# Kernel optimization log

Measured on AMD Instinct MI355X. Metric: run time of the kernel, lower is better.

Reference implementation:

```python
import jax, jax.numpy as jnp
import numpy as np

N_NODES = 200_000
N_EDGES = 6_400_000
N_GRAPHS = 512


def _sage_conv(x, edge_index, Wl, bl, Wr):
    """PyG SAGEConv (mean aggr): lin_l(mean_j x_j) + lin_r(x_i).
    lin_l has bias, lin_r does not. Messages flow src -> dst."""
    src, dst = edge_index[0], edge_index[1]
    n = x.shape[0]
    # gather neighbor features [E, F] and segment-mean into dst nodes
    msg_sum = jax.ops.segment_sum(x[src], dst, num_segments=n)
    deg = jax.ops.segment_sum(jnp.ones((src.shape[0],), x.dtype), dst, num_segments=n)
    mean = msg_sum / jnp.maximum(deg, 1.0)[:, None]  # zero in-degree -> 0
    return mean @ Wl.T + bl + x @ Wr.T


def setup_inputs() -> dict:
    key = jax.random.key(0)
    ks = jax.random.split(key, 9)
    x = jax.random.normal(ks[0], (N_NODES, 1), dtype=jnp.float32)
    edge_index = jax.random.randint(ks[1], (2, N_EDGES), 0, N_NODES, dtype=jnp.int64)
    batch = jnp.sort(jax.random.randint(ks[2], (N_NODES,), 0, N_GRAPHS, dtype=jnp.int64))
    W1l = jax.random.normal(ks[3], (16, 1), dtype=jnp.float32)
    b1 = jax.random.normal(ks[4], (16,), dtype=jnp.float32)
    W1r = jax.random.normal(ks[5], (16, 1), dtype=jnp.float32)
    W2l = jax.random.normal(ks[6], (1, 16), dtype=jnp.float32)
    b2 = jax.random.normal(ks[7], (1,), dtype=jnp.float32)
    W2r = jax.random.normal(ks[8], (1, 16), dtype=jnp.float32)
    return {"x": x, "edge_index": edge_index, "batch": batch, "batch_size": N_GRAPHS,
            "W1l": W1l, "b1": b1, "W1r": W1r, "W2l": W2l, "b2": b2, "W2r": W2r}


def reference(x, edge_index, batch, batch_size, W1l, b1, W1r, W2l, b2, W2r):
    h = _sage_conv(x, edge_index, W1l, b1, W1r)          # [N, 16]
    h = jax.nn.relu(h)
    h = _sage_conv(h, edge_index, W2l, b2, W2r)          # [N, 1]
    # global_add_pool: segment-sum node features by graph id
    out = jax.ops.segment_sum(h, batch, num_segments=batch_size)  # [B, 1]
    return out
```

## Files before the change

### kernel.cpp

```cpp
#include <hip/hip_runtime.h>


#define PP        16
#define BLK       1024
#define SCAP      1024u
#define SMASK     1023u
#define TILE      (BLK * 4)
#define CBIN      16
#define CNT_ONE   (1u << 25)
#define FX_BIAS   131072
#define SCALE     4096.0f
#define INV_SCALE (1.0f / 4096.0f)

__global__ __launch_bounds__(BLK) void partition_kernel(
    const int* __restrict__ ei, unsigned* __restrict__ pairs,
    unsigned* __restrict__ tails, int E, int bins, unsigned Mdiv, int cap) {
    extern __shared__ unsigned buf[];
    __shared__ unsigned cnt[PP], base[PP], fq[PP], gb[PP];
    const int tid = threadIdx.x;
    if (tid < PP) { cnt[tid] = 0; base[tid] = 0; }
    __syncthreads();

    int b0 = blockIdx.x * TILE;
    int e0 = b0 + tid * 4;
    int nv = E - e0; nv = nv < 0 ? 0 : (nv > 4 ? 4 : nv);
    int srcv[4], dstv[4];
    if (nv == 4 && ((E & 3) == 0)) {
        int4 s = *(const int4*)(ei + e0);
        int4 d = *(const int4*)(ei + E + e0);
        srcv[0] = s.x; srcv[1] = s.y; srcv[2] = s.z; srcv[3] = s.w;
        dstv[0] = d.x; dstv[1] = d.y; dstv[2] = d.z; dstv[3] = d.w;
    } else {
        for (int j = 0; j < nv; ++j) { srcv[j] = ei[e0 + j]; dstv[j] = ei[E + e0 + j]; }
    }
    unsigned w[4]; int part[4]; bool pend[4];
    for (int j = 0; j < 4; ++j) {
        pend[j] = (j < nv);
        if (pend[j]) {
            unsigned dst = (unsigned)dstv[j];
            unsigned pt = (unsigned)(((unsigned long long)dst * Mdiv) >> 32);
            int ld = (int)dst - (int)pt * bins;
            while (ld >= bins) { ld -= bins; ++pt; }
            while (ld < 0)     { ld += bins; --pt; }
            part[j] = (int)pt;
            w[j] = ((unsigned)srcv[j] << 14) | (unsigned)ld;
        }
    }
    for (int j = 0; j < 4; ++j) {
        if (pend[j]) {
            unsigned slot = atomicAdd(&cnt[part[j]], 1u);
            if (slot - base[part[j]] < SCAP) {
                buf[part[j] * SCAP + (slot & SMASK)] = w[j]; pend[j] = false;
            } else atomicSub(&cnt[part[j]], 1u);
        }
    }
    int npend = __syncthreads_count((int)(pend[0] | pend[1] | pend[2] | pend[3]));
    while (npend > 0) {
        if (tid < PP) {
            unsigned avail = cnt[tid] - base[tid];
            unsigned f = avail & ~511u;
            fq[tid] = f;
            if (f) gb[tid] = atomicAdd(&tails[tid], f);
        }
        __syncthreads();
        {
            int wv = tid >> 6, lane = tid & 63;
            unsigned f = fq[wv];
            if (f) {
                unsigned g0 = gb[wv], bs = base[wv];
                unsigned mx = (g0 + f <= (unsigned)cap) ? f : ((unsigned)cap > g0 ? (unsigned)cap - g0 : 0u);
                unsigned* dp = pairs + (size_t)wv * cap + g0;
                for (unsigned jj = lane; jj < mx; jj += 64)
                    dp[jj] = buf[wv * SCAP + ((bs + jj) & SMASK)];
            }
        }
        __syncthreads();
        if (tid < PP) base[tid] += fq[tid];
        __syncthreads();
        for (int j = 0; j < 4; ++j) {
            if (pend[j]) {
                unsigned slot = atomicAdd(&cnt[part[j]], 1u);
                if (slot - base[part[j]] < SCAP) {
                    buf[part[j] * SCAP + (slot & SMASK)] = w[j]; pend[j] = false;
                } else atomicSub(&cnt[part[j]], 1u);
            }
        }
        npend = __syncthreads_count((int)(pend[0] | pend[1] | pend[2] | pend[3]));
    }
    if (tid < PP) {
        unsigned avail = cnt[tid] - base[tid];
        fq[tid] = avail;
        if (avail) gb[tid] = atomicAdd(&tails[tid], avail);
    }
    __syncthreads();
    {
        int wv = tid >> 6, lane = tid & 63;
        unsigned f = fq[wv];
        if (f) {
            unsigned g0 = gb[wv], bs = base[wv];
            unsigned mx = (g0 + f <= (unsigned)cap) ? f : ((unsigned)cap > g0 ? (unsigned)cap - g0 : 0u);
            unsigned* dp = pairs + (size_t)wv * cap + g0;
            for (unsigned jj = lane; jj < mx; jj += 64)
                dp[jj] = buf[wv * SCAP + ((bs + jj) & SMASK)];
        }
    }
}

__global__ __launch_bounds__(BLK) void bin1_kernel(
    const unsigned* __restrict__ pairs, const unsigned* __restrict__ tails,
    const float* __restrict__ x, unsigned* __restrict__ slab,
    int N, int bins, int cap) {
    extern __shared__ unsigned sb[];
    int p = blockIdx.x & (PP - 1);
    int c = blockIdx.x / PP;
    int len = (int)tails[p]; if (len > cap) len = cap;
    int st = (int)((long long)len * c / CBIN);
    int en = (int)((long long)len * (c + 1) / CBIN);
    for (int j = threadIdx.x; j < bins; j += BLK) sb[j] = 0;
    __syncthreads();
    const unsigned* bp = pairs + (size_t)p * cap;
    int st4 = (st + 3) & ~3;
    int en4 = en & ~3;
    int preEnd = st4 < en ? st4 : en;
    for (int e = st + (int)threadIdx.x; e < preEnd; e += BLK) {
        unsigned wv = bp[e];
        atomicAdd(&sb[wv & 16383u],
                  CNT_ONE + (unsigned)((int)rintf(x[wv >> 14] * SCALE) + FX_BIAS));
    }
    if (st4 < en4) {
        const uint4* bp4 = (const uint4*)(bp + st4);
        int n4 = (en4 - st4) >> 2;
        for (int e = threadIdx.x; e < n4; e += BLK) {
            uint4 wq = bp4[e];
            atomicAdd(&sb[wq.x & 16383u],
                      CNT_ONE + (unsigned)((int)rintf(x[wq.x >> 14] * SCALE) + FX_BIAS));
            atomicAdd(&sb[wq.y & 16383u],
                      CNT_ONE + (unsigned)((int)rintf(x[wq.y >> 14] * SCALE) + FX_BIAS));
            atomicAdd(&sb[wq.z & 16383u],
                      CNT_ONE + (unsigned)((int)rintf(x[wq.z >> 14] * SCALE) + FX_BIAS));
            atomicAdd(&sb[wq.w & 16383u],
                      CNT_ONE + (unsigned)((int)rintf(x[wq.w >> 14] * SCALE) + FX_BIAS));
        }
    }
    int tailSt = st4 > en4 ? st4 : en4;
    for (int e = tailSt + (int)threadIdx.x; e < en; e += BLK) {
        unsigned wv = bp[e];
        atomicAdd(&sb[wv & 16383u],
                  CNT_ONE + (unsigned)((int)rintf(x[wv >> 14] * SCALE) + FX_BIAS));
    }
    __syncthreads();
    unsigned* dst = slab + (size_t)c * N + (size_t)p * bins;
    int nb = N - p * bins; if (nb > bins) nb = bins;
    for (int j = threadIdx.x; j < nb; j += BLK) dst[j] = sb[j];
}

__global__ __launch_bounds__(BLK) void bin2_kernel(
    const unsigned* __restrict__ pairs, const unsigned* __restrict__ tails,
    const float* __restrict__ pv, int* __restrict__ slab,
    int N, int bins, int cap) {
    extern __shared__ int sbi[];
    int p = blockIdx.x & (PP - 1);
    int c = blockIdx.x / PP;
    int len = (int)tails[p]; if (len > cap) len = cap;
    int st = (int)((long long)len * c / CBIN);
    int en = (int)((long long)len * (c + 1) / CBIN);
    for (int j = threadIdx.x; j < bins; j += BLK) sbi[j] = 0;
    __syncthreads();
    const unsigned* bp = pairs + (size_t)p * cap;
    int st4 = (st + 3) & ~3;
    int en4 = en & ~3;
    int preEnd = st4 < en ? st4 : en;
    for (int e = st + (int)threadIdx.x; e < preEnd; e += BLK) {
        unsigned wv = bp[e];
        atomicAdd(&sbi[wv & 16383u], (int)rintf(pv[wv >> 14] * SCALE));
    }
    if (st4 < en4) {
        const uint4* bp4 = (const uint4*)(bp + st4);
        int n4 = (en4 - st4) >> 2;
        for (int e = threadIdx.x; e < n4; e += BLK) {
            uint4 wq = bp4[e];
            atomicAdd(&sbi[wq.x & 16383u], (int)rintf(pv[wq.x >> 14] * SCALE));
            atomicAdd(&sbi[wq.y & 16383u], (int)rintf(pv[wq.y >> 14] * SCALE));
            atomicAdd(&sbi[wq.z & 16383u], (int)rintf(pv[wq.z >> 14] * SCALE));
            atomicAdd(&sbi[wq.w & 16383u], (int)rintf(pv[wq.w >> 14] * SCALE));
        }
    }
    int tailSt = st4 > en4 ? st4 : en4;
    for (int e = tailSt + (int)threadIdx.x; e < en; e += BLK) {
        unsigned wv = bp[e];
        atomicAdd(&sbi[wv & 16383u], (int)rintf(pv[wv >> 14] * SCALE));
    }
    __syncthreads();
    int* dst = slab + (size_t)c * N + (size_t)p * bins;
    int nb = N - p * bins; if (nb > bins) nb = bins;
    for (int j = threadIdx.x; j < nb; j += BLK) dst[j] = sbi[j];
}

__global__ void node_pass1_kernel(const float* __restrict__ x,
                                  const unsigned* __restrict__ slab,
                                  const float* __restrict__ W1l,
                                  const float* __restrict__ b1,
                                  const float* __restrict__ W1r,
                                  const float* __restrict__ W2l,
                                  const float* __restrict__ W2r,
                                  float* __restrict__ deg_out,
                                  float* __restrict__ pv,
                                  float* __restrict__ qv,
                                  int N) {
    __shared__ float s_w1l[16], s_b1[16], s_w1r[16], s_w2l[16], s_w2r[16];
    if (threadIdx.x < 16) {
        s_w1l[threadIdx.x] = W1l[threadIdx.x];
        s_b1[threadIdx.x]  = b1[threadIdx.x];
        s_w1r[threadIdx.x] = W1r[threadIdx.x];
        s_w2l[threadIdx.x] = W2l[threadIdx.x];
        s_w2r[threadIdx.x] = W2r[threadIdx.x];
    }
    __syncthreads();
    int n = blockIdx.x * blockDim.x + threadIdx.x;
    if (n >= N) return;

    unsigned cnt = 0, fx = 0;
#pragma unroll
    for (int c = 0; c < CBIN; ++c) {
        unsigned w = slab[(size_t)c * N + n];
        cnt += w >> 25;
        fx  += w & (CNT_ONE - 1);
    }
    float dg  = (float)cnt;
    float sum = (float)(int)(fx - cnt * (unsigned)FX_BIAS) * INV_SCALE;
    float m   = sum / fmaxf(dg, 1.0f);

    float xv = x[n];
    float pa = 0.0f, qa = 0.0f;
#pragma unroll
    for (int f = 0; f < 16; ++f) {
        float h = fmaf(m, s_w1l[f], fmaf(xv, s_w1r[f], s_b1[f]));
        h = fmaxf(h, 0.0f);
        pa = fmaf(h, s_w2l[f], pa);
        qa = fmaf(h, s_w2r[f], qa);
    }
    deg_out[n] = dg;
    pv[n] = pa;
    qv[n] = qa;
}

__global__ void node_pass2_kernel(const int* __restrict__ slab2,
                                  const float* __restrict__ deg,
                                  const float* __restrict__ qv,
                                  const float* __restrict__ b2,
                                  const int* __restrict__ batch,
                                  float* __restrict__ out,
                                  int N) {
    int i = blockIdx.x * blockDim.x + threadIdx.x;
    float b2v = b2[0];
    float val = 0.0f;
    int g;
    if (i < N) {
        int sacc = 0;
#pragma unroll
        for (int c = 0; c < CBIN; ++c) sacc += slab2[(size_t)c * N + i];
        float s2 = (float)sacc * INV_SCALE;
        val = s2 / fmaxf(deg[i], 1.0f) + b2v + qv[i];
        g = batch[i];
    } else {
        g = batch[N - 1];
    }
    int g0 = __shfl(g, 0);
    unsigned long long same = __ballot(g == g0);
    if (same == ~0ULL) {
        for (int off = 32; off > 0; off >>= 1) val += __shfl_down(val, off);
        if ((threadIdx.x & 63) == 0) atomicAdd(&out[g0], val);
    } else {
        atomicAdd(&out[g], val);
    }
}

extern "C" void kernel_launch(void* const* d_in, const int* in_sizes, int n_in,
                              void* d_out, int out_size, void* d_ws, size_t ws_size,
                              hipStream_t stream) {
    const float* x     = (const float*)d_in[0];
    const int*   ei    = (const int*)d_in[1];
    const int*   batch = (const int*)d_in[2];
    const float* W1l = (const float*)d_in[4];
    const float* b1  = (const float*)d_in[5];
    const float* W1r = (const float*)d_in[6];
    const float* W2l = (const float*)d_in[7];
    const float* b2  = (const float*)d_in[8];
    const float* W2r = (const float*)d_in[9];

    const int N = in_sizes[0];
    const int E = in_sizes[1] / 2;
    float* out = (float*)d_out;

    const int bins = (N + PP - 1) / PP;
    const unsigned Mdiv =
        (unsigned)(((1ULL << 32) + (unsigned)bins - 1) / (unsigned)bins);
    const int EperP = E / PP;
    int cap = ((EperP + EperP / 32 + 4096) + 1023) & ~1023;

    unsigned* pairs = (unsigned*)d_ws;
    unsigned* slab1 = pairs + (size_t)PP * cap;
    int*      slab2 = (int*)slab1;
    float* deg = (float*)(slab1 + (size_t)CBIN * N);
    float* pv  = deg + N;
    float* qv  = pv + N;
    unsigned* tails = (unsigned*)(qv + N);

    hipMemsetAsync(d_out, 0, (size_t)out_size * sizeof(float), stream);
    hipMemsetAsync(tails, 0, PP * sizeof(unsigned), stream);

    const int partShmem = PP * (int)SCAP * 4;
    const int binShmem  = bins * 4;
    hipFuncSetAttribute((const void*)partition_kernel,
                        hipFuncAttributeMaxDynamicSharedMemorySize, partShmem);
    hipFuncSetAttribute((const void*)bin1_kernel,
                        hipFuncAttributeMaxDynamicSharedMemorySize, binShmem);
    hipFuncSetAttribute((const void*)bin2_kernel,
                        hipFuncAttributeMaxDynamicSharedMemorySize, binShmem);

    int partBlocks = (E + TILE - 1) / TILE;
    const int NB = 256;
    int node_blocks = (N + NB - 1) / NB;

    partition_kernel<<<partBlocks, BLK, partShmem, stream>>>(ei, pairs, tails,
                                                             E, bins, Mdiv, cap);
    bin1_kernel<<<PP * CBIN, BLK, binShmem, stream>>>(pairs, tails, x, slab1,
                                                      N, bins, cap);
    node_pass1_kernel<<<node_blocks, NB, 0, stream>>>(x, slab1, W1l, b1, W1r,
                                                      W2l, W2r, deg, pv, qv, N);
    bin2_kernel<<<PP * CBIN, BLK, binShmem, stream>>>(pairs, tails, pv, slab2,
                                                      N, bins, cap);
    node_pass2_kernel<<<node_blocks, NB, 0, stream>>>(slab2, deg, qv, b2, batch,
                                                      out, N);
}
```

Measured before the change: 222.3 us.

## Add second-level source-range partition so bin kernels gather from shared memory

Adds a subpart kernel that splits each destination partition's edge list by source-node block of 8192, so bin1/bin2 can stage the x or pv slice in LDS and gather from shared memory instead of random global loads. The per-chunk slabs are replaced by a single accumulator that blocks update with global atomics, which removes the 16-way slab reduction in the node passes. The cost is an extra full pass over the edge pairs, a second buffer of pairs, and global atomic contention on the accumulators.

```diff
diff --git a/kernel.cpp b/kernel.cpp
--- a/kernel.cpp
+++ b/kernel.cpp
@@ -6,7 +6,10 @@
 #define SCAP      1024u
 #define SMASK     1023u
 #define TILE      (BLK * 4)
-#define CBIN      16
+#define SBW       8192
+#define SBSH      13
+#define SC2       512u
+#define SM2       511u
 #define CNT_ONE   (1u << 25)
 #define FX_BIAS   131072
 #define SCALE     4096.0f
@@ -106,98 +109,184 @@
     }
 }
 
+__global__ __launch_bounds__(BLK) void subpart_kernel(
+    const unsigned* __restrict__ pairsB, const unsigned* __restrict__ tails,
+    unsigned* __restrict__ pairsC, unsigned* __restrict__ tails2,
+    int NSB, int cap, int capSB) {
+    extern __shared__ unsigned buf[];
+    __shared__ unsigned cnt[32], base[32], fq[32], gb[32];
+    const int tid = threadIdx.x;
+    const int p = blockIdx.x & (PP - 1);
+    const int c = blockIdx.x >> 4;
+    if (tid < NSB) { cnt[tid] = 0; base[tid] = 0; }
+    __syncthreads();
+    int len = (int)tails[p]; if (len > cap) len = cap;
+    int st = (int)((long long)len * c / 16);
+    int en = (int)((long long)len * (c + 1) / 16);
+    const unsigned* bp = pairsB + (size_t)p * cap;
+    unsigned* cellbase = pairsC + (size_t)p * NSB * capSB;
+    unsigned* t2 = tails2 + (size_t)p * NSB;
+
+    for (int e0 = st; e0 < en; e0 += BLK * 4) {
+        unsigned w[4]; int sb[4]; bool pend[4];
+        for (int j = 0; j < 4; ++j) {
+            int e = e0 + tid + j * BLK;
+            pend[j] = e < en;
+            if (pend[j]) {
+                unsigned wv = bp[e];
+                unsigned src = wv >> 14;
+                sb[j] = (int)(src >> SBSH);
+                w[j] = ((src & (SBW - 1u)) << 14) | (wv & 16383u);
+            }
+        }
+        for (int j = 0; j < 4; ++j) {
+            if (pend[j]) {
+                unsigned slot = atomicAdd(&cnt[sb[j]], 1u);
+                if (slot - base[sb[j]] < SC2) {
+                    buf[sb[j] * SC2 + (slot & SM2)] = w[j]; pend[j] = false;
+                } else atomicSub(&cnt[sb[j]], 1u);
+            }
+        }
+        int npend = __syncthreads_count((int)(pend[0] | pend[1] | pend[2] | pend[3]));
+        while (npend > 0) {
+            if (tid < NSB) {
+                unsigned avail = cnt[tid] - base[tid];
+                unsigned f = avail & ~255u;
+                fq[tid] = f;
+                if (f) gb[tid] = atomicAdd(&t2[tid], f);
+            }
+            __syncthreads();
+            for (int r = tid >> 6; r < NSB; r += 16) {
+                int lane = tid & 63;
+                unsigned f = fq[r];
+                if (f) {
+                    unsigned g0 = gb[r], bs = base[r];
+                    unsigned mx = (g0 + f <= (unsigned)capSB) ? f : ((unsigned)capSB > g0 ? (unsigned)capSB - g0 : 0u);
+                    unsigned* dp = cellbase + (size_t)r * capSB + g0;
+                    for (unsigned jj = lane; jj < mx; jj += 64)
+                        dp[jj] = buf[r * SC2 + ((bs + jj) & SM2)];
+                }
+            }
+            __syncthreads();
+            if (tid < NSB) base[tid] += fq[tid];
+            __syncthreads();
+            for (int j = 0; j < 4; ++j) {
+                if (pend[j]) {
+                    unsigned slot = atomicAdd(&cnt[sb[j]], 1u);
+                    if (slot - base[sb[j]] < SC2) {
+                        buf[sb[j] * SC2 + (slot & SM2)] = w[j]; pend[j] = false;
+                    } else atomicSub(&cnt[sb[j]], 1u);
+                }
+            }
+            npend = __syncthreads_count((int)(pend[0] | pend[1] | pend[2] | pend[3]));
+        }
+    }
+    if (tid < NSB) {
+        unsigned avail = cnt[tid] - base[tid];
+        fq[tid] = avail;
+        if (avail) gb[tid] = atomicAdd(&t2[tid], avail);
+    }
+    __syncthreads();
+    for (int r = tid >> 6; r < NSB; r += 16) {
+        int lane = tid & 63;
+        unsigned f = fq[r];
+        if (f) {
+            unsigned g0 = gb[r], bs = base[r];
+            unsigned mx = (g0 + f <= (unsigned)capSB) ? f : ((unsigned)capSB > g0 ? (unsigned)capSB - g0 : 0u);
+            unsigned* dp = cellbase + (size_t)r * capSB + g0;
+            for (unsigned jj = lane; jj < mx; jj += 64)
+                dp[jj] = buf[r * SC2 + ((bs + jj) & SM2)];
+        }
+    }
+}
+
 __global__ __launch_bounds__(BLK) void bin1_kernel(
-    const unsigned* __restrict__ pairs, const unsigned* __restrict__ tails,
-    const float* __restrict__ x, unsigned* __restrict__ slab,
-    int N, int bins, int cap) {
-    extern __shared__ unsigned sb[];
-    int p = blockIdx.x & (PP - 1);
-    int c = blockIdx.x / PP;
-    int len = (int)tails[p]; if (len > cap) len = cap;
-    int st = (int)((long long)len * c / CBIN);
-    int en = (int)((long long)len * (c + 1) / CBIN);
-    for (int j = threadIdx.x; j < bins; j += BLK) sb[j] = 0;
-    __syncthreads();
-    const unsigned* bp = pairs + (size_t)p * cap;
-    int st4 = (st + 3) & ~3;
-    int en4 = en & ~3;
-    int preEnd = st4 < en ? st4 : en;
-    for (int e = st + (int)threadIdx.x; e < preEnd; e += BLK) {
+    const unsigned* __restrict__ pairsC, const unsigned* __restrict__ tails2,
+    const float* __restrict__ x, unsigned* __restrict__ acc1,
+    int N, int bins, int NSB, int capSB) {
+    extern __shared__ unsigned sm[];
+    float* xs = (float*)sm;
+    unsigned* sbn = sm + SBW;
+    const int tid = threadIdx.x;
+    const int cell = blockIdx.x;
+    const int p = cell / NSB;
+    const int sbk = cell - p * NSB;
+    const int n0 = sbk << SBSH;
+    int nn = N - n0; if (nn > SBW) nn = SBW;
+    for (int j = tid; j < nn; j += BLK) xs[j] = x[n0 + j];
+    for (int j = tid; j < bins; j += BLK) sbn[j] = 0;
+    __syncthreads();
+    int len = (int)tails2[cell]; if (len > capSB) len = capSB;
+    const unsigned* bp = pairsC + (size_t)cell * capSB;
+    int len4 = len & ~3;
+    const uint4* bp4 = (const uint4*)bp;
+    for (int e = tid; e < (len4 >> 2); e += BLK) {
+        uint4 wq = bp4[e];
+        atomicAdd(&sbn[wq.x & 16383u],
+                  CNT_ONE + (unsigned)((int)rintf(xs[wq.x >> 14] * SCALE) + FX_BIAS));
+        atomicAdd(&sbn[wq.y & 16383u],
+                  CNT_ONE + (unsigned)((int)rintf(xs[wq.y >> 14] * SCALE) + FX_BIAS));
+        atomicAdd(&sbn[wq.z & 16383u],
+                  CNT_ONE + (unsigned)((int)rintf(xs[wq.z >> 14] * SCALE) + FX_BIAS));
+        atomicAdd(&sbn[wq.w & 16383u],
+                  CNT_ONE + (unsigned)((int)rintf(xs[wq.w >> 14] * SCALE) + FX_BIAS));
+    }
+    for (int e = len4 + tid; e < len; e += BLK) {
         unsigned wv = bp[e];
-        atomicAdd(&sb[wv & 16383u],
-                  CNT_ONE + (unsigned)((int)rintf(x[wv >> 14] * SCALE) + FX_BIAS));
-    }
-    if (st4 < en4) {
-        const uint4* bp4 = (const uint4*)(bp + st4);
-        int n4 = (en4 - st4) >> 2;
-        for (int e = threadIdx.x; e < n4; e += BLK) {
-            uint4 wq = bp4[e];
-            atomicAdd(&sb[wq.x & 16383u],
-                      CNT_ONE + (unsigned)((int)rintf(x[wq.x >> 14] * SCALE) + FX_BIAS));
-            atomicAdd(&sb[wq.y & 16383u],
-                      CNT_ONE + (unsigned)((int)rintf(x[wq.y >> 14] * SCALE) + FX_BIAS));
-            atomicAdd(&sb[wq.z & 16383u],
-                      CNT_ONE + (unsigned)((int)rintf(x[wq.z >> 14] * SCALE) + FX_BIAS));
-            atomicAdd(&sb[wq.w & 16383u],
-                      CNT_ONE + (unsigned)((int)rintf(x[wq.w >> 14] * SCALE) + FX_BIAS));
-        }
-    }
-    int tailSt = st4 > en4 ? st4 : en4;
-    for (int e = tailSt + (int)threadIdx.x; e < en; e += BLK) {
+        atomicAdd(&sbn[wv & 16383u],
+                  CNT_ONE + (unsigned)((int)rintf(xs[wv >> 14] * SCALE) + FX_BIAS));
+    }
+    __syncthreads();
+    unsigned* dst = acc1 + (size_t)p * bins;
+    int nb = N - p * bins; if (nb > bins) nb = bins;
+    for (int j = tid; j < nb; j += BLK) {
+        unsigned v = sbn[j];
+        if (v) atomicAdd(&dst[j], v);
+    }
+}
+
+__global__ __launch_bounds__(BLK) void bin2_kernel(
+    const unsigned* __restrict__ pairsC, const unsigned* __restrict__ tails2,
+    const float* __restrict__ pv, int* __restrict__ acc2,
+    int N, int bins, int NSB, int capSB) {
+    extern __shared__ unsigned sm[];
+    float* ps = (float*)sm;
+    int* sbi = (int*)(sm + SBW);
+    const int tid = threadIdx.x;
+    const int cell = blockIdx.x;
+    const int p = cell / NSB;
+    const int sbk = cell - p * NSB;
+    const int n0 = sbk << SBSH;
+    int nn = N - n0; if (nn > SBW) nn = SBW;
+    for (int j = tid; j < nn; j += BLK) ps[j] = pv[n0 + j];
+    for (int j = tid; j < bins; j += BLK) sbi[j] = 0;
+    __syncthreads();
+    int len = (int)tails2[cell]; if (len > capSB) len = capSB;
+    const unsigned* bp = pairsC + (size_t)cell * capSB;
+    int len4 = len & ~3;
+    const uint4* bp4 = (const uint4*)bp;
+    for (int e = tid; e < (len4 >> 2); e += BLK) {
+        uint4 wq = bp4[e];
+        atomicAdd(&sbi[wq.x & 16383u], (int)rintf(ps[wq.x >> 14] * SCALE));
+        atomicAdd(&sbi[wq.y & 16383u], (int)rintf(ps[wq.y >> 14] * SCALE));
+        atomicAdd(&sbi[wq.z & 16383u], (int)rintf(ps[wq.z >> 14] * SCALE));
+        atomicAdd(&sbi[wq.w & 16383u], (int)rintf(ps[wq.w >> 14] * SCALE));
+    }
+    for (int e = len4 + tid; e < len; e += BLK) {
         unsigned wv = bp[e];
-        atomicAdd(&sb[wv & 16383u],
-                  CNT_ONE + (unsigned)((int)rintf(x[wv >> 14] * SCALE) + FX_BIAS));
-    }
-    __syncthreads();
-    unsigned* dst = slab + (size_t)c * N + (size_t)p * bins;
+        atomicAdd(&sbi[wv & 16383u], (int)rintf(ps[wv >> 14] * SCALE));
+    }
+    __syncthreads();
+    int* dst = acc2 + (size_t)p * bins;
     int nb = N - p * bins; if (nb > bins) nb = bins;
-    for (int j = threadIdx.x; j < nb; j += BLK) dst[j] = sb[j];
-}
-
-__global__ __launch_bounds__(BLK) void bin2_kernel(
-    const unsigned* __restrict__ pairs, const unsigned* __restrict__ tails,
-    const float* __restrict__ pv, int* __restrict__ slab,
-    int N, int bins, int cap) {
-    extern __shared__ int sbi[];
-    int p = blockIdx.x & (PP - 1);
-    int c = blockIdx.x / PP;
-    int len = (int)tails[p]; if (len > cap) len = cap;
-    int st = (int)((long long)len * c / CBIN);
-    int en = (int)((long long)len * (c + 1) / CBIN);
-    for (int j = threadIdx.x; j < bins; j += BLK) sbi[j] = 0;
-    __syncthreads();
-    const unsigned* bp = pairs + (size_t)p * cap;
-    int st4 = (st + 3) & ~3;
-    int en4 = en & ~3;
-    int preEnd = st4 < en ? st4 : en;
-    for (int e = st + (int)threadIdx.x; e < preEnd; e += BLK) {
-        unsigned wv = bp[e];
-        atomicAdd(&sbi[wv & 16383u], (int)rintf(pv[wv >> 14] * SCALE));
-    }
-    if (st4 < en4) {
-        const uint4* bp4 = (const uint4*)(bp + st4);
-        int n4 = (en4 - st4) >> 2;
-        for (int e = threadIdx.x; e < n4; e += BLK) {
-            uint4 wq = bp4[e];
-            atomicAdd(&sbi[wq.x & 16383u], (int)rintf(pv[wq.x >> 14] * SCALE));
-            atomicAdd(&sbi[wq.y & 16383u], (int)rintf(pv[wq.y >> 14] * SCALE));
-            atomicAdd(&sbi[wq.z & 16383u], (int)rintf(pv[wq.z >> 14] * SCALE));
-            atomicAdd(&sbi[wq.w & 16383u], (int)rintf(pv[wq.w >> 14] * SCALE));
-        }
-    }
-    int tailSt = st4 > en4 ? st4 : en4;
-    for (int e = tailSt + (int)threadIdx.x; e < en; e += BLK) {
-        unsigned wv = bp[e];
-        atomicAdd(&sbi[wv & 16383u], (int)rintf(pv[wv >> 14] * SCALE));
-    }
-    __syncthreads();
-    int* dst = slab + (size_t)c * N + (size_t)p * bins;
-    int nb = N - p * bins; if (nb > bins) nb = bins;
-    for (int j = threadIdx.x; j < nb; j += BLK) dst[j] = sbi[j];
+    for (int j = tid; j < nb; j += BLK) {
+        int v = sbi[j];
+        if (v) atomicAdd(&dst[j], v);
+    }
 }
 
 __global__ void node_pass1_kernel(const float* __restrict__ x,
-                                  const unsigned* __restrict__ slab,
+                                  const unsigned* __restrict__ acc1,
                                   const float* __restrict__ W1l,
                                   const float* __restrict__ b1,
                                   const float* __restrict__ W1r,
@@ -219,13 +308,9 @@
     int n = blockIdx.x * blockDim.x + threadIdx.x;
     if (n >= N) return;
 
-    unsigned cnt = 0, fx = 0;
-#pragma unroll
-    for (int c = 0; c < CBIN; ++c) {
-        unsigned w = slab[(size_t)c * N + n];
-        cnt += w >> 25;
-        fx  += w & (CNT_ONE - 1);
-    }
+    unsigned w = acc1[n];
+    unsigned cnt = w >> 25;
+    unsigned fx  = w & (CNT_ONE - 1);
     float dg  = (float)cnt;
     float sum = (float)(int)(fx - cnt * (unsigned)FX_BIAS) * INV_SCALE;
     float m   = sum / fmaxf(dg, 1.0f);
@@ -244,7 +329,7 @@
     qv[n] = qa;
 }
 
-__global__ void node_pass2_kernel(const int* __restrict__ slab2,
+__global__ void node_pass2_kernel(const int* __restrict__ acc2,
                                   const float* __restrict__ deg,
                                   const float* __restrict__ qv,
                                   const float* __restrict__ b2,
@@ -256,10 +341,7 @@
     float val = 0.0f;
     int g;
     if (i < N) {
-        int sacc = 0;
-#pragma unroll
-        for (int c = 0; c < CBIN; ++c) sacc += slab2[(size_t)c * N + i];
-        float s2 = (float)sacc * INV_SCALE;
+        float s2 = (float)acc2[i] * INV_SCALE;
         val = s2 / fmaxf(deg[i], 1.0f) + b2v + qv[i];
         g = batch[i];
     } else {
@@ -293,26 +375,34 @@
     float* out = (float*)d_out;
 
     const int bins = (N + PP - 1) / PP;
+    const int NSB  = (N + SBW - 1) / SBW;
     const unsigned Mdiv =
         (unsigned)(((1ULL << 32) + (unsigned)bins - 1) / (unsigned)bins);
     const int EperP = E / PP;
     int cap = ((EperP + EperP / 32 + 4096) + 1023) & ~1023;
-
-    unsigned* pairs = (unsigned*)d_ws;
-    unsigned* slab1 = pairs + (size_t)PP * cap;
-    int*      slab2 = (int*)slab1;
-    float* deg = (float*)(slab1 + (size_t)CBIN * N);
+    const int meanSB = E / (PP * NSB);
+    int capSB = ((meanSB + meanSB / 4 + 2048) + 1023) & ~1023;
+
+    unsigned* pairsB = (unsigned*)d_ws;
+    unsigned* pairsC = pairsB + (size_t)PP * cap;
+    unsigned* acc1   = pairsC + (size_t)PP * NSB * capSB;
+    int*      acc2   = (int*)(acc1 + N);
+    unsigned* tails  = (unsigned*)(acc2 + N);
+    unsigned* tails2 = tails + PP;
+    float* deg = (float*)(tails2 + (size_t)PP * NSB);
     float* pv  = deg + N;
     float* qv  = pv + N;
-    unsigned* tails = (unsigned*)(qv + N);
 
     hipMemsetAsync(d_out, 0, (size_t)out_size * sizeof(float), stream);
-    hipMemsetAsync(tails, 0, PP * sizeof(unsigned), stream);
+    hipMemsetAsync(acc1, 0, (size_t)(2 * N + PP + PP * NSB) * 4, stream);
 
     const int partShmem = PP * (int)SCAP * 4;
-    const int binShmem  = bins * 4;
+    const int subShmem  = NSB * (int)SC2 * 4;
+    const int binShmem  = SBW * 4 + bins * 4;
     hipFuncSetAttribute((const void*)partition_kernel,
                         hipFuncAttributeMaxDynamicSharedMemorySize, partShmem);
+    hipFuncSetAttribute((const void*)subpart_kernel,
+                        hipFuncAttributeMaxDynamicSharedMemorySize, subShmem);
     hipFuncSetAttribute((const void*)bin1_kernel,
                         hipFuncAttributeMaxDynamicSharedMemorySize, binShmem);
     hipFuncSetAttribute((const void*)bin2_kernel,
@@ -322,14 +412,16 @@
     const int NB = 256;
     int node_blocks = (N + NB - 1) / NB;
 
-    partition_kernel<<<partBlocks, BLK, partShmem, stream>>>(ei, pairs, tails,
+    partition_kernel<<<partBlocks, BLK, partShmem, stream>>>(ei, pairsB, tails,
                                                              E, bins, Mdiv, cap);
-    bin1_kernel<<<PP * CBIN, BLK, binShmem, stream>>>(pairs, tails, x, slab1,
-                                                      N, bins, cap);
-    node_pass1_kernel<<<node_blocks, NB, 0, stream>>>(x, slab1, W1l, b1, W1r,
+    subpart_kernel<<<PP * 16, BLK, subShmem, stream>>>(pairsB, tails, pairsC,
+                                                       tails2, NSB, cap, capSB);
+    bin1_kernel<<<PP * NSB, BLK, binShmem, stream>>>(pairsC, tails2, x, acc1,
+                                                     N, bins, NSB, capSB);
+    node_pass1_kernel<<<node_blocks, NB, 0, stream>>>(x, acc1, W1l, b1, W1r,
                                                       W2l, W2r, deg, pv, qv, N);
-    bin2_kernel<<<PP * CBIN, BLK, binShmem, stream>>>(pairs, tails, pv, slab2,
-                                                      N, bins, cap);
-    node_pass2_kernel<<<node_blocks, NB, 0, stream>>>(slab2, deg, qv, b2, batch,
+    bin2_kernel<<<PP * NSB, BLK, binShmem, stream>>>(pairsC, tails2, pv, acc2,
+                                                     N, bins, NSB, capSB);
+    node_pass2_kernel<<<node_blocks, NB, 0, stream>>>(acc2, deg, qv, b2, batch,
                                                       out, N);
 }
```

After: 229.4 us. 3.2% more time.
